# Kernel tuning notes

Hardware: AMD Instinct MI355X
Metric: run time of the kernel (lower is better)

Reference implementation:

```python
import jax, jax.numpy as jnp
import numpy as np

N, E = 50000, 1600000
IN_DIM, HID, HEADS, DH, NCLS = 1280, 256, 4, 64, 6
NEG_SLOPE = 0.2
LN_EPS = 1e-5


def setup_inputs() -> dict:
    key = jax.random.key(0)
    ks = jax.random.split(key, 24)
    p = {}
    p['x'] = jax.random.normal(ks[0], (N, IN_DIM), dtype=jnp.float32)
    p['edge_index'] = jax.random.randint(ks[1], (2, E), 0, N, dtype=jnp.int64)
    s = 0.05
    p['W_in'] = jax.random.normal(ks[2], (IN_DIM, HID), dtype=jnp.float32) * s
    p['b_in'] = jnp.zeros((HID,), jnp.float32)
    for l in range(2):
        p[f'W_gat{l}'] = jax.random.normal(ks[3 + 6 * l], (HID, HEADS * DH), dtype=jnp.float32) * s
        p[f'att_src{l}'] = jax.random.normal(ks[4 + 6 * l], (HEADS, DH), dtype=jnp.float32) * s
        p[f'att_dst{l}'] = jax.random.normal(ks[5 + 6 * l], (HEADS, DH), dtype=jnp.float32) * s
        p[f'b_gat{l}'] = jnp.zeros((HEADS * DH,), jnp.float32)
        p[f'ln_g{l}'] = jnp.ones((HID,), jnp.float32)
        p[f'ln_b{l}'] = jnp.zeros((HID,), jnp.float32)
    p['W_c1'] = jax.random.normal(ks[20], (HID, HID // 2), dtype=jnp.float32) * s
    p['b_c1'] = jnp.zeros((HID // 2,), jnp.float32)
    p['W_c2'] = jax.random.normal(ks[21], (HID // 2, NCLS), dtype=jnp.float32) * s
    p['b_c2'] = jnp.zeros((NCLS,), jnp.float32)
    return p


def _layer_norm(h, g, b):
    mu = jnp.mean(h, axis=-1, keepdims=True)
    var = jnp.mean((h - mu) ** 2, axis=-1, keepdims=True)
    return (h - mu) * jax.lax.rsqrt(var + LN_EPS) * g + b


def _gat_conv(h, src, dst, W, a_src, a_dst, bias):
    # h: [N, HID] -> per-head projections [N, H, DH]
    xh = (h @ W).reshape(N, HEADS, DH)
    al_src = jnp.sum(xh * a_src, axis=-1)  # [N, H]
    al_dst = jnp.sum(xh * a_dst, axis=-1)  # [N, H]
    e = jax.nn.leaky_relu(al_src[src] + al_dst[dst], NEG_SLOPE)  # [E', H]
    # edge softmax over incoming edges of each destination node
    m = jax.ops.segment_max(e, dst, num_segments=N)
    e = jnp.exp(e - m[dst])
    denom = jax.ops.segment_sum(e, dst, num_segments=N)
    w = e / denom[dst]  # [E', H]
    msg = xh[src] * w[:, :, None]  # [E', H, DH]
    out = jax.ops.segment_sum(msg, dst, num_segments=N)  # [N, H, DH]
    return out.reshape(N, HEADS * DH) + bias


def reference(x, edge_index, W_in, b_in, W_gat0, att_src0, att_dst0, b_gat0, ln_g0, ln_b0,
              W_gat1, att_src1, att_dst1, b_gat1, ln_g1, ln_b1, W_c1, b_c1, W_c2, b_c2):
    # add self loops (PyG GATConv default)
    loop = jnp.arange(N, dtype=edge_index.dtype)
    src = jnp.concatenate([edge_index[0], loop])
    dst = jnp.concatenate([edge_index[1], loop])

    h = jax.nn.relu(x @ W_in + b_in)

    for (Wg, asrc, adst, bg, g, b) in ((W_gat0, att_src0, att_dst0, b_gat0, ln_g0, ln_b0),
                                       (W_gat1, att_src1, att_dst1, b_gat1, ln_g1, ln_b1)):
        h_new = _gat_conv(h, src, dst, Wg, asrc, adst, bg)
        h_new = jax.nn.relu(_layer_norm(h_new, g, b))
        h = h + h_new

    logits = jax.nn.relu(h @ W_c1 + b_c1) @ W_c2 + b_c2
    return logits
```

## Files before the change

### kernel.cpp

```cpp
#include <hip/hip_runtime.h>

#define NN 50000
#define EE 1600000
#define INDIM 1280
#define HID 256
#define HEADS 4
#define DHD 64
#define NCLS 6
#define NEG 0.2f
#define LNEPS 1e-5f

typedef __attribute__((ext_vector_type(8))) short short8;
typedef __attribute__((ext_vector_type(4))) float floatx4;

__device__ __forceinline__ unsigned short f2b(float f) {
    unsigned int u = __float_as_uint(f);
    u += 0x7FFF + ((u >> 16) & 1);
    return (unsigned short)(u >> 16);
}
__device__ __forceinline__ float b2f(unsigned short b) {
    return __uint_as_float(((unsigned int)b) << 16);
}

#define WAIT_LGKM0() __builtin_amdgcn_s_waitcnt(0xC07F)

__global__ void init_cnt_kernel(int* __restrict__ cnt) {
    int n = blockIdx.x * 256 + threadIdx.x;
    if (n < NN) cnt[n] = 1;
}

__global__ void count_edges_kernel(const int* __restrict__ dst, int* __restrict__ cnt) {
    int e = blockIdx.x * 256 + threadIdx.x;
    if (e < EE) atomicAdd(&cnt[dst[e]], 1);
}

__global__ __launch_bounds__(1024) void scan1_kernel(const int* __restrict__ cnt,
                                                     int* __restrict__ scanned,
                                                     int* __restrict__ chtot, int n) {
    __shared__ int wsum[16];
    int tid = threadIdx.x, lane = tid & 63, wv = tid >> 6;
    int i = blockIdx.x * 1024 + tid;
    int s = (i < n) ? cnt[i] : 0;
#pragma unroll
    for (int off = 1; off < 64; off <<= 1) {
        int t = __shfl_up(s, off, 64);
        if (lane >= off) s += t;
    }
    if (lane == 63) wsum[wv] = s;
    __syncthreads();
    if (tid < 16) {
        int ws = wsum[tid];
#pragma unroll
        for (int off = 1; off < 16; off <<= 1) {
            int t = __shfl_up(ws, off, 16);
            if (tid >= off) ws += t;
        }
        wsum[tid] = ws;
    }
    __syncthreads();
    s += (wv > 0) ? wsum[wv - 1] : 0;
    if (i < n) scanned[i] = s;
    if (tid == 1023) chtot[blockIdx.x] = s;
}

__global__ void scan2_kernel(int* __restrict__ chtot, int nch) {
    int lane = threadIdx.x;
    int v = (lane < nch) ? chtot[lane] : 0;
#pragma unroll
    for (int off = 1; off < 64; off <<= 1) {
        int t = __shfl_up(v, off, 64);
        if (lane >= off) v += t;
    }
    if (lane < nch) chtot[lane] = v;
}

__global__ void scan3_kernel(const int* __restrict__ scanned, const int* __restrict__ chtot,
                             int* __restrict__ rowptr, int n) {
    int i = blockIdx.x * 256 + threadIdx.x;
    if (i == 0) rowptr[0] = 0;
    if (i < n) {
        int ch = i >> 10;
        rowptr[i + 1] = scanned[i] + (ch ? chtot[ch - 1] : 0);
    }
}

__global__ void copyfill_kernel(const int* __restrict__ rowptr, int* __restrict__ cursor,
                                int* __restrict__ csr) {
    int n = blockIdx.x * 256 + threadIdx.x;
    if (n < NN) {
        int p = rowptr[n];
        csr[p] = n;
        cursor[n] = p + 1;
    }
}

__global__ void scatter_edges_kernel(const int* __restrict__ src, const int* __restrict__ dst,
                                     int* __restrict__ cursor, int* __restrict__ csr) {
    int e = blockIdx.x * 256 + threadIdx.x;
    if (e < EE) {
        int d = dst[e];
        int pos = atomicAdd(&cursor[d], 1);
        csr[pos] = src[e];
    }
}

__global__ void pack_w_kernel(const float* __restrict__ W, unsigned short* __restrict__ out,
                              int K, int N) {
    int idx = blockIdx.x * 256 + threadIdx.x;
    int total = (K >> 6) * (N >> 4) * 2 * 64;
    if (idx >= total) return;
    int ln = idx & 63;
    int t = idx >> 6;
    int ks = t & 1; t >>= 1;
    int NT = N >> 4;
    int nt = t % NT, kc = t / NT;
    int n = nt * 16 + (ln & 15);
    int k = kc * 64 + ks * 32 + ((ln >> 4) << 3);
    unsigned short u[8];
#pragma unroll
    for (int j = 0; j < 8; j++) u[j] = f2b(W[(size_t)(k + j) * N + n]);
    *(int4*)&out[(size_t)idx * 8] = *(const int4*)u;
}

template <int AF32, int KI, int NT, int ACT, int WF32, int WB16>
__global__ __launch_bounds__(256) void pgemm_kernel(const float* __restrict__ Af,
                                                    const unsigned short* __restrict__ Ab,
                                                    const unsigned short* __restrict__ Bf,
                                                    const float* __restrict__ bias,
                                                    float* __restrict__ Cf,
                                                    unsigned short* __restrict__ Cb,
                                                    int M) {
    constexpr int NW = NT / 4;
    constexpr int K = KI * 64;
    __shared__ __align__(16) unsigned short Als[2][4096];
    int tid = threadIdx.x, wv = tid >> 6, ln = tid & 63;
    int m0 = blockIdx.x * 64;

    int srow[2], scol[2];
#pragma unroll
    for (int i = 0; i < 2; i++) {
        int s = tid + i * 256;
        int r = s >> 3;
        srow[i] = min(m0 + r, M - 1);
        scol[i] = ((s & 7) ^ (r & 7)) * 8;
    }

    floatx4 acc[4][NW] = {};
    short8 breg[2][NW * 2];
    float4 af0[4], af1[4];
    int4 ai0[2], ai1[2];

    auto issueA = [&](int k, float4* af, int4* ai) {
#pragma unroll
        for (int i = 0; i < 2; i++) {
            if (AF32) {
                const float* p = Af + (size_t)srow[i] * K + k * 64 + scol[i];
                af[i * 2] = *(const float4*)p;
                af[i * 2 + 1] = *(const float4*)(p + 4);
            } else {
                ai[i] = *(const int4*)(Ab + (size_t)srow[i] * K + k * 64 + scol[i]);
            }
        }
    };
    auto issueB = [&](int k, short8* b) {
#pragma unroll
        for (int nw = 0; nw < NW; nw++)
#pragma unroll
            for (int ks = 0; ks < 2; ks++)
                b[nw * 2 + ks] = *(const short8*)(
                    Bf + ((((size_t)k * NT + (wv * NW + nw)) * 2 + ks) * 64 + ln) * 8);
    };
    auto writeA = [&](int k, const float4* af, const int4* ai) {
        unsigned short* dst = &Als[k & 1][0];
#pragma unroll
        for (int i = 0; i < 2; i++) {
            int4 v;
            if (AF32) {
                unsigned short u[8] = {f2b(af[2 * i].x), f2b(af[2 * i].y),
                                       f2b(af[2 * i].z), f2b(af[2 * i].w),
                                       f2b(af[2 * i + 1].x), f2b(af[2 * i + 1].y),
                                       f2b(af[2 * i + 1].z), f2b(af[2 * i + 1].w)};
                v = *(const int4*)u;
            } else {
                v = ai[i];
            }
            *(int4*)&dst[(tid + i * 256) * 8] = v;
        }
    };
    auto compute = [&](int k, const short8* b) {
        const unsigned short* src = &Als[k & 1][0];
#pragma unroll
        for (int ks = 0; ks < 2; ks++) {
            short8 a[4];
#pragma unroll
            for (int mt = 0; mt < 4; mt++) {
                int row = mt * 16 + (ln & 15);
                int g = ks * 4 + (ln >> 4);
                int off8 = (row >> 3) * 512 + (row & 7) * 64 + (g ^ (row & 7)) * 8;
                a[mt] = *(const short8*)&src[off8];
            }
#pragma unroll
            for (int nw = 0; nw < NW; nw++)
#pragma unroll
                for (int mt = 0; mt < 4; mt++)
                    acc[mt][nw] = __builtin_amdgcn_mfma_f32_16x16x32_bf16(
                        a[mt], b[nw * 2 + ks], acc[mt][nw], 0, 0, 0);
        }
    };

    issueA(0, af0, ai0);
    issueB(0, breg[0]);
    writeA(0, af0, ai0);
    WAIT_LGKM0();
    __builtin_amdgcn_s_barrier();

#pragma unroll
    for (int kk = 0; kk < KI / 2; kk++) {
        int k = kk * 2;
        issueA(k + 1, af1, ai1);
        issueB(k + 1, breg[1]);
        compute(k, breg[0]);
        writeA(k + 1, af1, ai1);
        WAIT_LGKM0();
        __builtin_amdgcn_s_barrier();
        if (k + 2 < KI) {
            issueA(k + 2, af0, ai0);
            issueB(k + 2, breg[0]);
        }
        compute(k + 1, breg[1]);
        if (k + 2 < KI) {
            writeA(k + 2, af0, ai0);
            WAIT_LGKM0();
            __builtin_amdgcn_s_barrier();
        }
    }

    constexpr int Nout = NT * 16;
#pragma unroll
    for (int mt = 0; mt < 4; mt++) {
#pragma unroll
        for (int nw = 0; nw < NW; nw++) {
            int col = (wv * NW + nw) * 16 + (ln & 15);
            int rb = m0 + mt * 16 + (ln >> 4) * 4;
            float bi = bias ? bias[col] : 0.f;
#pragma unroll
            for (int r = 0; r < 4; r++) {
                int row = rb + r;
                if (row < M) {
                    float v = acc[mt][nw][r] + bi;
                    if (ACT) v = fmaxf(v, 0.f);
                    if (WF32) Cf[(size_t)row * Nout + col] = v;
                    if (WB16) Cb[(size_t)row * Nout + col] = f2b(v);
                }
            }
        }
    }
}

__global__ __launch_bounds__(256) void proj_al_kernel(const unsigned short* __restrict__ xhb,
                                                      const float* __restrict__ a_src,
                                                      const float* __restrict__ a_dst,
                                                      float* __restrict__ al_s,
                                                      float* __restrict__ al_d) {
    int n = blockIdx.x * 4 + (threadIdx.x >> 6);
    if (n >= NN) return;
    int lane = threadIdx.x & 63;
    ushort4 v4 = ((const ushort4*)(xhb + (size_t)n * HID))[lane];
    int base = lane * 4;
    float4 as4 = *(const float4*)&a_src[base];
    float4 ad4 = *(const float4*)&a_dst[base];
    float x0 = b2f(v4.x), x1 = b2f(v4.y), x2 = b2f(v4.z), x3 = b2f(v4.w);
    float ps = x0 * as4.x + x1 * as4.y + x2 * as4.z + x3 * as4.w;
    float pd = x0 * ad4.x + x1 * ad4.y + x2 * ad4.z + x3 * ad4.w;
#pragma unroll
    for (int off = 8; off > 0; off >>= 1) {
        ps += __shfl_down(ps, off, 16);
        pd += __shfl_down(pd, off, 16);
    }
    if ((lane & 15) == 0) {
        int h = lane >> 4;
        al_s[n * 4 + h] = ps;
        al_d[n * 4 + h] = pd;
    }
}

__global__ __launch_bounds__(256) void agg_ln_kernel(const int* __restrict__ rowptr,
                                                     const int* __restrict__ csr,
                                                     const float* __restrict__ al_s,
                                                     const float* __restrict__ al_d,
                                                     const unsigned short* __restrict__ xhb,
                                                     const float* __restrict__ bgat,
                                                     const float* __restrict__ g,
                                                     const float* __restrict__ bb,
                                                     float* __restrict__ h,
                                                     unsigned short* __restrict__ hb) {
    int wv = threadIdx.x >> 6, ln = threadIdx.x & 63;
    int n = blockIdx.x * 4 + wv;
    if (n >= NN) return;
    int start = rowptr[n], end = rowptr[n + 1];
    float4 ad = *(const float4*)&al_d[n * 4];

    float d0 = 0.f, d1 = 0.f, d2 = 0.f, d3 = 0.f;
    for (int i = start + ln; i < end; i += 64) {
        int s = csr[i];
        float4 as = *(const float4*)&al_s[s * 4];
        float e0 = as.x + ad.x; e0 = e0 > 0.f ? e0 : NEG * e0;
        float e1 = as.y + ad.y; e1 = e1 > 0.f ? e1 : NEG * e1;
        float e2 = as.z + ad.z; e2 = e2 > 0.f ? e2 : NEG * e2;
        float e3 = as.w + ad.w; e3 = e3 > 0.f ? e3 : NEG * e3;
        d0 += __expf(e0); d1 += __expf(e1); d2 += __expf(e2); d3 += __expf(e3);
    }
#pragma unroll
    for (int off = 32; off > 0; off >>= 1) {
        d0 += __shfl_xor(d0, off, 64);
        d1 += __shfl_xor(d1, off, 64);
        d2 += __shfl_xor(d2, off, 64);
        d3 += __shfl_xor(d3, off, 64);
    }
    int myh = ln >> 4;
    float invh = 1.f / ((myh == 0) ? d0 : (myh == 1) ? d1 : (myh == 2) ? d2 : d3);
    float adh = (myh == 0) ? ad.x : (myh == 1) ? ad.y : (myh == 2) ? ad.z : ad.w;

    float a0 = 0.f, a1 = 0.f, a2 = 0.f, a3 = 0.f;
#pragma unroll 2
    for (int i = start; i < end; i++) {
        int s = csr[i];
        float e = al_s[s * 4 + myh] + adh;
        e = e > 0.f ? e : NEG * e;
        float w = __expf(e) * invh;
        ushort4 mv = *(const ushort4*)&xhb[(size_t)s * HID + ln * 4];
        a0 = fmaf(w, b2f(mv.x), a0);
        a1 = fmaf(w, b2f(mv.y), a1);
        a2 = fmaf(w, b2f(mv.z), a2);
        a3 = fmaf(w, b2f(mv.w), a3);
    }

    float4 bg = *(const float4*)&bgat[ln * 4];
    float v0 = a0 + bg.x, v1 = a1 + bg.y, v2 = a2 + bg.z, v3 = a3 + bg.w;
    float ps = v0 + v1 + v2 + v3;
    float ps2 = v0 * v0 + v1 * v1 + v2 * v2 + v3 * v3;
#pragma unroll
    for (int off = 32; off > 0; off >>= 1) {
        ps += __shfl_xor(ps, off, 64);
        ps2 += __shfl_xor(ps2, off, 64);
    }
    float mu = ps * (1.f / HID);
    float var = ps2 * (1.f / HID) - mu * mu;
    float rs = rsqrtf(var + LNEPS);
    float4 gg = *(const float4*)&g[ln * 4];
    float4 bbv = *(const float4*)&bb[ln * 4];
    float o0 = fmaxf((v0 - mu) * rs * gg.x + bbv.x, 0.f);
    float o1 = fmaxf((v1 - mu) * rs * gg.y + bbv.y, 0.f);
    float o2 = fmaxf((v2 - mu) * rs * gg.z + bbv.z, 0.f);
    float o3 = fmaxf((v3 - mu) * rs * gg.w + bbv.w, 0.f);
    size_t idx = (size_t)n * HID + ln * 4;
    float4 hv = *(const float4*)&h[idx];
    float4 nh = make_float4(hv.x + o0, hv.y + o1, hv.z + o2, hv.w + o3);
    *(float4*)&h[idx] = nh;
    ushort4 nb = {f2b(nh.x), f2b(nh.y), f2b(nh.z), f2b(nh.w)};
    *(ushort4*)&hb[idx] = nb;
}

__global__ void cls2_kernel(const float* __restrict__ mid, const float* __restrict__ W,
                            const float* __restrict__ bias, float* __restrict__ out) {
    int idx = blockIdx.x * 256 + threadIdx.x;
    if (idx >= NN * NCLS) return;
    int n = idx / NCLS, c = idx % NCLS;
    const float* row = mid + (size_t)n * (HID / 2);
    float acc = bias[c];
#pragma unroll 8
    for (int k = 0; k < HID / 2; k++) acc += row[k] * W[k * NCLS + c];
    out[idx] = acc;
}

extern "C" void kernel_launch(void* const* d_in, const int* in_sizes, int n_in,
                              void* d_out, int out_size, void* d_ws, size_t ws_size,
                              hipStream_t stream) {
    const float* x    = (const float*)d_in[0];
    const int*   ei   = (const int*)d_in[1];
    const float* W_in = (const float*)d_in[2];
    const float* b_in = (const float*)d_in[3];
    const float* W_gat[2]   = {(const float*)d_in[4],  (const float*)d_in[10]};
    const float* att_src[2] = {(const float*)d_in[5],  (const float*)d_in[11]};
    const float* att_dst[2] = {(const float*)d_in[6],  (const float*)d_in[12]};
    const float* b_gat[2]   = {(const float*)d_in[7],  (const float*)d_in[13]};
    const float* ln_g[2]    = {(const float*)d_in[8],  (const float*)d_in[14]};
    const float* ln_b[2]    = {(const float*)d_in[9],  (const float*)d_in[15]};
    const float* W_c1 = (const float*)d_in[16];
    const float* b_c1 = (const float*)d_in[17];
    const float* W_c2 = (const float*)d_in[18];
    const float* b_c2 = (const float*)d_in[19];

    char* ws = (char*)d_ws;
    size_t off = 0;
    auto alloc = [&](size_t bytes) -> void* {
        void* p = ws + off;
        off += (bytes + 255) & ~(size_t)255;
        return p;
    };
    float*          h   = (float*)alloc((size_t)NN * HID * 4);
    unsigned short* hb  = (unsigned short*)alloc((size_t)NN * HID * 2);
    unsigned short* xhb = (unsigned short*)alloc((size_t)NN * HID * 2);
    float* al_s = (float*)alloc((size_t)NN * HEADS * 4);
    float* al_d = (float*)alloc((size_t)NN * HEADS * 4);
    int* rowptr  = (int*)alloc((size_t)(NN + 1) * 4);
    int* cursor  = (int*)alloc((size_t)NN * 4);
    int* csr     = (int*)alloc((size_t)(EE + NN) * 4);
    int* scanned = (int*)alloc((size_t)NN * 4);
    int* chtot   = (int*)alloc(64 * 4);
    unsigned short* WinF = (unsigned short*)alloc((size_t)HID * INDIM * 2);
    unsigned short* WgF0 = (unsigned short*)alloc((size_t)HID * HID * 2);
    unsigned short* WgF1 = (unsigned short*)alloc((size_t)HID * HID * 2);
    unsigned short* Wc1F = (unsigned short*)alloc((size_t)(HID / 2) * HID * 2);
    unsigned short* WgF[2] = {WgF0, WgF1};
    float* mid = (float*)xhb;

    const int* srcv = ei;
    const int* dstv = ei + EE;

    pack_w_kernel<<<(INDIM * HID / 8 + 255) / 256, 256, 0, stream>>>(W_in, WinF, INDIM, HID);
    pack_w_kernel<<<(HID * HID / 8 + 255) / 256, 256, 0, stream>>>(W_gat[0], WgF0, HID, HID);
    pack_w_kernel<<<(HID * HID / 8 + 255) / 256, 256, 0, stream>>>(W_gat[1], WgF1, HID, HID);
    pack_w_kernel<<<(HID * (HID / 2) / 8 + 255) / 256, 256, 0, stream>>>(W_c1, Wc1F, HID, HID / 2);

    int nch = (NN + 1023) / 1024;
    init_cnt_kernel<<<(NN + 255) / 256, 256, 0, stream>>>(cursor);
    count_edges_kernel<<<(EE + 255) / 256, 256, 0, stream>>>(dstv, cursor);
    scan1_kernel<<<nch, 1024, 0, stream>>>(cursor, scanned, chtot, NN);
    scan2_kernel<<<1, 64, 0, stream>>>(chtot, nch);
    scan3_kernel<<<(NN + 255) / 256, 256, 0, stream>>>(scanned, chtot, rowptr, NN);
    copyfill_kernel<<<(NN + 255) / 256, 256, 0, stream>>>(rowptr, cursor, csr);
    scatter_edges_kernel<<<(EE + 255) / 256, 256, 0, stream>>>(srcv, dstv, cursor, csr);

    int MB64 = (NN + 63) / 64;

    pgemm_kernel<1, 20, 16, 1, 1, 1><<<MB64, 256, 0, stream>>>(
        x, nullptr, WinF, b_in, h, hb, NN);

    for (int l = 0; l < 2; l++) {
        pgemm_kernel<0, 4, 16, 0, 0, 1><<<MB64, 256, 0, stream>>>(
            nullptr, hb, WgF[l], nullptr, nullptr, xhb, NN);
        proj_al_kernel<<<(NN + 3) / 4, 256, 0, stream>>>(xhb, att_src[l], att_dst[l], al_s, al_d);
        agg_ln_kernel<<<(NN + 3) / 4, 256, 0, stream>>>(rowptr, csr, al_s, al_d, xhb,
                                                        b_gat[l], ln_g[l], ln_b[l], h, hb);
    }

    pgemm_kernel<0, 4, 8, 1, 1, 0><<<MB64, 256, 0, stream>>>(
        nullptr, hb, Wc1F, b_c1, mid, nullptr, NN);
    cls2_kernel<<<(NN * NCLS + 255) / 256, 256, 0, stream>>>(mid, W_c2, b_c2, (float*)d_out);
}
```

Baseline: 1.039 ms.

## Fuse attention-logit projection and classifier head into GEMM epilogues; unroll aggregation

The per-node attention dot products (al_s/al_d) now come straight from the GEMM accumulators in the GAT projection epilogue, which removes the separate proj_al kernel and its re-read of xhb. The final classifier layer is also fused into the Wc1 GEMM epilogue. It reduces across heads through shared memory, so the fp32 intermediate buffer and the cls2 kernel are no longer needed. The aggregation loop is manually unrolled by two with independent accumulators to raise memory-level parallelism. In exchange, the attention logits are computed from fp32 accumulators instead of bf16-rounded values, and the epilogues use more registers.

```diff
diff --git a/kernel.cpp b/kernel.cpp
--- a/kernel.cpp
+++ b/kernel.cpp
@@ -122,13 +122,20 @@
     *(int4*)&out[(size_t)idx * 8] = *(const int4*)u;
 }
 
-template <int AF32, int KI, int NT, int ACT, int WF32, int WB16>
+template <int AF32, int KI, int NT, int ACT, int WF32, int WB16, int PROJ, int CLS>
 __global__ __launch_bounds__(256) void pgemm_kernel(const float* __restrict__ Af,
                                                     const unsigned short* __restrict__ Ab,
                                                     const unsigned short* __restrict__ Bf,
                                                     const float* __restrict__ bias,
                                                     float* __restrict__ Cf,
                                                     unsigned short* __restrict__ Cb,
+                                                    const float* __restrict__ aps,
+                                                    const float* __restrict__ apd,
+                                                    float* __restrict__ als,
+                                                    float* __restrict__ ald,
+                                                    const float* __restrict__ W2,
+                                                    const float* __restrict__ b2,
+                                                    float* __restrict__ out2,
                                                     int M) {
     constexpr int NW = NT / 4;
     constexpr int K = KI * 64;
@@ -236,51 +243,101 @@
     }
 
     constexpr int Nout = NT * 16;
-#pragma unroll
-    for (int mt = 0; mt < 4; mt++) {
+    if constexpr (WF32 || WB16) {
+#pragma unroll
+        for (int mt = 0; mt < 4; mt++) {
+#pragma unroll
+            for (int nw = 0; nw < NW; nw++) {
+                int col = (wv * NW + nw) * 16 + (ln & 15);
+                int rb = m0 + mt * 16 + (ln >> 4) * 4;
+                float bi = bias ? bias[col] : 0.f;
+#pragma unroll
+                for (int r = 0; r < 4; r++) {
+                    int row = rb + r;
+                    if (row < M) {
+                        float v = acc[mt][nw][r] + bi;
+                        if (ACT) v = fmaxf(v, 0.f);
+                        if (WF32) Cf[(size_t)row * Nout + col] = v;
+                        if (WB16) Cb[(size_t)row * Nout + col] = f2b(v);
+                    }
+                }
+            }
+        }
+    }
+
+    if constexpr (PROJ) {
+        float avs[NW], avd[NW];
+#pragma unroll
+        for (int nw = 0; nw < NW; nw++) {
+            int d = nw * 16 + (ln & 15);
+            avs[nw] = aps[wv * DHD + d];
+            avd[nw] = apd[wv * DHD + d];
+        }
+#pragma unroll
+        for (int mt = 0; mt < 4; mt++) {
+#pragma unroll
+            for (int r = 0; r < 4; r++) {
+                float ssum = 0.f, dsum = 0.f;
+#pragma unroll
+                for (int nw = 0; nw < NW; nw++) {
+                    float v = acc[mt][nw][r];
+                    ssum = fmaf(v, avs[nw], ssum);
+                    dsum = fmaf(v, avd[nw], dsum);
+                }
+#pragma unroll
+                for (int m = 8; m > 0; m >>= 1) {
+                    ssum += __shfl_xor(ssum, m, 16);
+                    dsum += __shfl_xor(dsum, m, 16);
+                }
+                int row = m0 + mt * 16 + (ln >> 4) * 4 + r;
+                if ((ln & 15) == 0 && row < M) {
+                    als[row * 4 + wv] = ssum;
+                    ald[row * 4 + wv] = dsum;
+                }
+            }
+        }
+    }
+
+    if constexpr (CLS) {
+        __shared__ float cred[64][4][NCLS];
+        float w2[NW][NCLS];
 #pragma unroll
         for (int nw = 0; nw < NW; nw++) {
             int col = (wv * NW + nw) * 16 + (ln & 15);
-            int rb = m0 + mt * 16 + (ln >> 4) * 4;
-            float bi = bias ? bias[col] : 0.f;
+#pragma unroll
+            for (int c = 0; c < NCLS; c++) w2[nw][c] = W2[col * NCLS + c];
+        }
+#pragma unroll
+        for (int mt = 0; mt < 4; mt++) {
 #pragma unroll
             for (int r = 0; r < 4; r++) {
-                int row = rb + r;
-                if (row < M) {
-                    float v = acc[mt][nw][r] + bi;
-                    if (ACT) v = fmaxf(v, 0.f);
-                    if (WF32) Cf[(size_t)row * Nout + col] = v;
-                    if (WB16) Cb[(size_t)row * Nout + col] = f2b(v);
+                float p[NCLS] = {};
+#pragma unroll
+                for (int nw = 0; nw < NW; nw++) {
+                    int col = (wv * NW + nw) * 16 + (ln & 15);
+                    float v = fmaxf(acc[mt][nw][r] + bias[col], 0.f);
+#pragma unroll
+                    for (int c = 0; c < NCLS; c++) p[c] = fmaf(v, w2[nw][c], p[c]);
                 }
-            }
-        }
-    }
-}
-
-__global__ __launch_bounds__(256) void proj_al_kernel(const unsigned short* __restrict__ xhb,
-                                                      const float* __restrict__ a_src,
-                                                      const float* __restrict__ a_dst,
-                                                      float* __restrict__ al_s,
-                                                      float* __restrict__ al_d) {
-    int n = blockIdx.x * 4 + (threadIdx.x >> 6);
-    if (n >= NN) return;
-    int lane = threadIdx.x & 63;
-    ushort4 v4 = ((const ushort4*)(xhb + (size_t)n * HID))[lane];
-    int base = lane * 4;
-    float4 as4 = *(const float4*)&a_src[base];
-    float4 ad4 = *(const float4*)&a_dst[base];
-    float x0 = b2f(v4.x), x1 = b2f(v4.y), x2 = b2f(v4.z), x3 = b2f(v4.w);
-    float ps = x0 * as4.x + x1 * as4.y + x2 * as4.z + x3 * as4.w;
-    float pd = x0 * ad4.x + x1 * ad4.y + x2 * ad4.z + x3 * ad4.w;
-#pragma unroll
-    for (int off = 8; off > 0; off >>= 1) {
-        ps += __shfl_down(ps, off, 16);
-        pd += __shfl_down(pd, off, 16);
-    }
-    if ((lane & 15) == 0) {
-        int h = lane >> 4;
-        al_s[n * 4 + h] = ps;
-        al_d[n * 4 + h] = pd;
+#pragma unroll
+                for (int m = 8; m > 0; m >>= 1)
+#pragma unroll
+                    for (int c = 0; c < NCLS; c++) p[c] += __shfl_xor(p[c], m, 16);
+                int rl = mt * 16 + (ln >> 4) * 4 + r;
+                if ((ln & 15) == 0)
+#pragma unroll
+                    for (int c = 0; c < NCLS; c++) cred[rl][wv][c] = p[c];
+            }
+        }
+        __syncthreads();
+        for (int t = tid; t < 64 * NCLS; t += 256) {
+            int row = t / NCLS, c = t % NCLS;
+            if (m0 + row < M) {
+                float s = cred[row][0][c] + cred[row][1][c] + cred[row][2][c] +
+                          cred[row][3][c] + b2[c];
+                out2[(size_t)(m0 + row) * NCLS + c] = s;
+            }
+        }
     }
 }
 
@@ -321,19 +378,33 @@
     float invh = 1.f / ((myh == 0) ? d0 : (myh == 1) ? d1 : (myh == 2) ? d2 : d3);
     float adh = (myh == 0) ? ad.x : (myh == 1) ? ad.y : (myh == 2) ? ad.z : ad.w;
 
-    float a0 = 0.f, a1 = 0.f, a2 = 0.f, a3 = 0.f;
-#pragma unroll 2
-    for (int i = start; i < end; i++) {
-        int s = csr[i];
-        float e = al_s[s * 4 + myh] + adh;
-        e = e > 0.f ? e : NEG * e;
-        float w = __expf(e) * invh;
-        ushort4 mv = *(const ushort4*)&xhb[(size_t)s * HID + ln * 4];
-        a0 = fmaf(w, b2f(mv.x), a0);
-        a1 = fmaf(w, b2f(mv.y), a1);
-        a2 = fmaf(w, b2f(mv.z), a2);
-        a3 = fmaf(w, b2f(mv.w), a3);
-    }
+    float p0 = 0.f, p1 = 0.f, p2 = 0.f, p3 = 0.f;
+    float q0 = 0.f, q1 = 0.f, q2 = 0.f, q3 = 0.f;
+    int i = start;
+    for (; i + 1 < end; i += 2) {
+        int s0 = csr[i], s1 = csr[i + 1];
+        float e0 = al_s[s0 * 4 + myh] + adh; e0 = e0 > 0.f ? e0 : NEG * e0;
+        float e1 = al_s[s1 * 4 + myh] + adh; e1 = e1 > 0.f ? e1 : NEG * e1;
+        float w0 = __expf(e0) * invh;
+        float w1 = __expf(e1) * invh;
+        ushort4 u0 = *(const ushort4*)&xhb[(size_t)s0 * HID + ln * 4];
+        ushort4 u1 = *(const ushort4*)&xhb[(size_t)s1 * HID + ln * 4];
+        p0 = fmaf(w0, b2f(u0.x), p0); q0 = fmaf(w1, b2f(u1.x), q0);
+        p1 = fmaf(w0, b2f(u0.y), p1); q1 = fmaf(w1, b2f(u1.y), q1);
+        p2 = fmaf(w0, b2f(u0.z), p2); q2 = fmaf(w1, b2f(u1.z), q2);
+        p3 = fmaf(w0, b2f(u0.w), p3); q3 = fmaf(w1, b2f(u1.w), q3);
+    }
+    if (i < end) {
+        int s0 = csr[i];
+        float e0 = al_s[s0 * 4 + myh] + adh; e0 = e0 > 0.f ? e0 : NEG * e0;
+        float w0 = __expf(e0) * invh;
+        ushort4 u0 = *(const ushort4*)&xhb[(size_t)s0 * HID + ln * 4];
+        p0 = fmaf(w0, b2f(u0.x), p0);
+        p1 = fmaf(w0, b2f(u0.y), p1);
+        p2 = fmaf(w0, b2f(u0.z), p2);
+        p3 = fmaf(w0, b2f(u0.w), p3);
+    }
+    float a0 = p0 + q0, a1 = p1 + q1, a2 = p2 + q2, a3 = p3 + q3;
 
     float4 bg = *(const float4*)&bgat[ln * 4];
     float v0 = a0 + bg.x, v1 = a1 + bg.y, v2 = a2 + bg.z, v3 = a3 + bg.w;
@@ -359,18 +430,6 @@
     *(float4*)&h[idx] = nh;
     ushort4 nb = {f2b(nh.x), f2b(nh.y), f2b(nh.z), f2b(nh.w)};
     *(ushort4*)&hb[idx] = nb;
-}
-
-__global__ void cls2_kernel(const float* __restrict__ mid, const float* __restrict__ W,
-                            const float* __restrict__ bias, float* __restrict__ out) {
-    int idx = blockIdx.x * 256 + threadIdx.x;
-    if (idx >= NN * NCLS) return;
-    int n = idx / NCLS, c = idx % NCLS;
-    const float* row = mid + (size_t)n * (HID / 2);
-    float acc = bias[c];
-#pragma unroll 8
-    for (int k = 0; k < HID / 2; k++) acc += row[k] * W[k * NCLS + c];
-    out[idx] = acc;
 }
 
 extern "C" void kernel_launch(void* const* d_in, const int* in_sizes, int n_in,
@@ -413,7 +472,6 @@
     unsigned short* WgF1 = (unsigned short*)alloc((size_t)HID * HID * 2);
     unsigned short* Wc1F = (unsigned short*)alloc((size_t)(HID / 2) * HID * 2);
     unsigned short* WgF[2] = {WgF0, WgF1};
-    float* mid = (float*)xhb;
 
     const int* srcv = ei;
     const int* dstv = ei + EE;
@@ -434,18 +492,19 @@
 
     int MB64 = (NN + 63) / 64;
 
-    pgemm_kernel<1, 20, 16, 1, 1, 1><<<MB64, 256, 0, stream>>>(
-        x, nullptr, WinF, b_in, h, hb, NN);
+    pgemm_kernel<1, 20, 16, 1, 1, 1, 0, 0><<<MB64, 256, 0, stream>>>(
+        x, nullptr, WinF, b_in, h, hb,
+        nullptr, nullptr, nullptr, nullptr, nullptr, nullptr, nullptr, NN);
 
     for (int l = 0; l < 2; l++) {
-        pgemm_kernel<0, 4, 16, 0, 0, 1><<<MB64, 256, 0, stream>>>(
-            nullptr, hb, WgF[l], nullptr, nullptr, xhb, NN);
-        proj_al_kernel<<<(NN + 3) / 4, 256, 0, stream>>>(xhb, att_src[l], att_dst[l], al_s, al_d);
+        pgemm_kernel<0, 4, 16, 0, 0, 1, 1, 0><<<MB64, 256, 0, stream>>>(
+            nullptr, hb, WgF[l], nullptr, nullptr, xhb,
+            att_src[l], att_dst[l], al_s, al_d, nullptr, nullptr, nullptr, NN);
         agg_ln_kernel<<<(NN + 3) / 4, 256, 0, stream>>>(rowptr, csr, al_s, al_d, xhb,
                                                         b_gat[l], ln_g[l], ln_b[l], h, hb);
     }
 
-    pgemm_kernel<0, 4, 8, 1, 1, 0><<<MB64, 256, 0, stream>>>(
-        nullptr, hb, Wc1F, b_c1, mid, nullptr, NN);
-    cls2_kernel<<<(NN * NCLS + 255) / 256, 256, 0, stream>>>(mid, W_c2, b_c2, (float*)d_out);
-}
+    pgemm_kernel<0, 4, 8, 1, 0, 0, 0, 1><<<MB64, 256, 0, stream>>>(
+        nullptr, hb, Wc1F, b_c1, nullptr, nullptr,
+        nullptr, nullptr, nullptr, nullptr, W_c2, b_c2, (float*)d_out, NN);
+}
```

New measurement: 1.011 ms. 2.7% less time.
